# Kernel optimization log

Measured on AMD Instinct MI355X. Metric: run time of the kernel, lower is better.

## Reference

```python
import jax, jax.numpy as jnp
import numpy as np

EMBED_DIM = 512
NUM_HEADS = 8
HEAD_DIM = EMBED_DIM // NUM_HEADS
SCALE = HEAD_DIM ** -0.5


def setup_inputs() -> dict:
    key = jax.random.key(0)
    ks = jax.random.split(key, 12)
    B, Nq, Nk, C = 2, 2048, 2048, EMBED_DIM
    # xavier_uniform bound for square CxC weights
    bound = float(np.sqrt(6.0 / (C + C)))
    def w(k):
        return jax.random.uniform(k, (C, C), jnp.float32, -bound, bound)
    return {
        "query": jax.random.normal(ks[0], (B, Nq, C), jnp.float32),
        "key": jax.random.normal(ks[1], (B, Nk, C), jnp.float32),
        "value": jax.random.normal(ks[2], (B, Nk, C), jnp.float32),
        "key_padding_mask": jnp.zeros((B, Nk), dtype=bool),
        "Wq": w(ks[3]), "bq": jnp.zeros((C,), jnp.float32),
        "Wk": w(ks[4]), "bk": jnp.zeros((C,), jnp.float32),
        "Wv": w(ks[5]), "bv": jnp.zeros((C,), jnp.float32),
        "Wo": w(ks[6]), "bo": jnp.zeros((C,), jnp.float32),
    }


def reference(query, key, value, key_padding_mask, Wq, bq, Wk, bk, Wv, bv, Wo, bo):
    B, Nq, C = query.shape
    Nk = key.shape[1]
    H, D = NUM_HEADS, HEAD_DIM
    # torch Linear: x @ W.T + b
    Q = (query @ Wq.T + bq).reshape(B, Nq, H, D).transpose(0, 2, 1, 3)  # (B,H,Nq,D)
    K = (key @ Wk.T + bk).reshape(B, Nk, H, D).transpose(0, 2, 1, 3)
    V = (value @ Wv.T + bv).reshape(B, Nk, H, D).transpose(0, 2, 1, 3)
    scores = jnp.einsum("bhqd,bhkd->bhqk", Q, K) * SCALE  # (B,H,Nq,Nk)
    scores = jnp.where(key_padding_mask[:, None, None, :], -jnp.inf, scores)
    attn = jax.nn.softmax(scores, axis=-1)
    out = jnp.einsum("bhqk,bhkd->bhqd", attn, V)  # (B,H,Nq,D)
    out = out.transpose(0, 2, 1, 3).reshape(B, Nq, C)
    return out @ Wo.T + bo
```

## Files before the change

### kernel.cpp

```cpp
#include <hip/hip_runtime.h>

typedef unsigned short u16;
typedef __attribute__((ext_vector_type(8))) short short8;
typedef __attribute__((ext_vector_type(8))) __bf16 bf16x8;
typedef __attribute__((ext_vector_type(4))) float f32x4;
typedef __attribute__((ext_vector_type(4))) unsigned int u32x4;

#define MFMA_BF16(a, b, c) __builtin_amdgcn_mfma_f32_16x16x32_bf16((a), (b), (c), 0, 0, 0)

__device__ __forceinline__ u16 f2bf(float f) {
    unsigned u = __builtin_bit_cast(unsigned, f);
    u += 0x7FFFu + ((u >> 16) & 1u);
    return (u16)(u >> 16);
}

__device__ __forceinline__ unsigned cvt_pk_bf16(float lo, float hi) {
    unsigned r;
    asm("v_cvt_pk_bf16_f32 %0, %1, %2" : "=v"(r) : "v"(lo), "v"(hi));
    return r;
}

__device__ __forceinline__ float fast_exp2(float x) {
    float r;
    asm("v_exp_f32 %0, %1" : "=v"(r) : "v"(x));
    return r;
}

__global__ __launch_bounds__(256) void proj_gemm(
    const float* __restrict__ Xq, const float* __restrict__ Xk, const float* __restrict__ Xv,
    const float* __restrict__ Wq, const float* __restrict__ Wk, const float* __restrict__ Wv,
    const float* __restrict__ bq, const float* __restrict__ bk, const float* __restrict__ bv,
    u16* __restrict__ Oq, u16* __restrict__ Ok, u16* __restrict__ Ov)
{
    constexpr int K = 512, N = 512;
    const int z = blockIdx.z;
    const float* __restrict__ X = (z == 0) ? Xq : (z == 1) ? Xk : Xv;
    const float* __restrict__ W = (z == 0) ? Wq : (z == 1) ? Wk : Wv;
    const float* __restrict__ bias = (z == 0) ? bq : (z == 1) ? bk : bv;
    u16* __restrict__ O = (z == 0) ? Oq : (z == 1) ? Ok : Ov;
    const float alpha = (z == 0) ? 0.125f * 1.44269504088896f : 1.0f;

    __shared__ u16 lA[128 * 64];
    __shared__ u16 lB[128 * 64];

    const int tid = threadIdx.x, lane = tid & 63, w = tid >> 6;
    const int wr = w >> 1, wc = w & 1;
    const int bm = blockIdx.x, bn = blockIdx.y;
    const int r0 = tid >> 3, cc = tid & 7;

    f32x4 acc[4][4];
    for (int m = 0; m < 4; ++m)
        for (int n = 0; n < 4; ++n)
            acc[m][n] = f32x4{0.f, 0.f, 0.f, 0.f};

    for (int kt = 0; kt < K; kt += 64) {
        __syncthreads();
        for (int p = 0; p < 4; ++p) {
            int r = r0 + p * 32;
            {
                const float4* g = (const float4*)(X + (size_t)(bm * 128 + r) * K + kt + cc * 8);
                float4 f0 = g[0], f1 = g[1];
                short8 v;
                v[0] = (short)f2bf(f0.x); v[1] = (short)f2bf(f0.y);
                v[2] = (short)f2bf(f0.z); v[3] = (short)f2bf(f0.w);
                v[4] = (short)f2bf(f1.x); v[5] = (short)f2bf(f1.y);
                v[6] = (short)f2bf(f1.z); v[7] = (short)f2bf(f1.w);
                *(short8*)&lA[r * 64 + ((cc ^ (r & 7)) << 3)] = v;
            }
            {
                const float4* g = (const float4*)(W + (size_t)(bn * 128 + r) * K + kt + cc * 8);
                float4 f0 = g[0], f1 = g[1];
                short8 v;
                v[0] = (short)f2bf(f0.x); v[1] = (short)f2bf(f0.y);
                v[2] = (short)f2bf(f0.z); v[3] = (short)f2bf(f0.w);
                v[4] = (short)f2bf(f1.x); v[5] = (short)f2bf(f1.y);
                v[6] = (short)f2bf(f1.z); v[7] = (short)f2bf(f1.w);
                *(short8*)&lB[r * 64 + ((cc ^ (r & 7)) << 3)] = v;
            }
        }
        __syncthreads();
        for (int kk = 0; kk < 2; ++kk) {
            bf16x8 af[4], bfr[4];
            for (int m = 0; m < 4; ++m) {
                int row = wr * 64 + m * 16 + (lane & 15);
                af[m] = *(const bf16x8*)&lA[row * 64 + (((kk * 4 + (lane >> 4)) ^ (row & 7)) << 3)];
            }
            for (int n = 0; n < 4; ++n) {
                int row = wc * 64 + n * 16 + (lane & 15);
                bfr[n] = *(const bf16x8*)&lB[row * 64 + (((kk * 4 + (lane >> 4)) ^ (row & 7)) << 3)];
            }
            for (int m = 0; m < 4; ++m)
                for (int n = 0; n < 4; ++n)
                    acc[m][n] = MFMA_BF16(af[m], bfr[n], acc[m][n]);
        }
    }
    for (int m = 0; m < 4; ++m)
        for (int n = 0; n < 4; ++n) {
            int row = bm * 128 + wr * 64 + m * 16 + ((lane >> 4) << 2);
            int col = bn * 128 + wc * 64 + n * 16 + (lane & 15);
            float bv_ = bias[col];
            for (int i = 0; i < 4; ++i) {
                float v = (acc[m][n][i] + bv_) * alpha;
                O[(size_t)(row + i) * N + col] = f2bf(v);
            }
        }
}

__global__ __launch_bounds__(256) void out_gemm(
    const u16* __restrict__ A, const float* __restrict__ W,
    const float* __restrict__ bias, float* __restrict__ O)
{
    constexpr int K = 512, N = 512;
    __shared__ u16 lA[128 * 64];
    __shared__ u16 lB[128 * 64];

    const int tid = threadIdx.x, lane = tid & 63, w = tid >> 6;
    const int wr = w >> 1, wc = w & 1;
    const int bm = blockIdx.x, bn = blockIdx.y;
    const int r0 = tid >> 3, cc = tid & 7;

    f32x4 acc[4][4];
    for (int m = 0; m < 4; ++m)
        for (int n = 0; n < 4; ++n)
            acc[m][n] = f32x4{0.f, 0.f, 0.f, 0.f};

    for (int kt = 0; kt < K; kt += 64) {
        __syncthreads();
        for (int p = 0; p < 4; ++p) {
            int r = r0 + p * 32;
            *(short8*)&lA[r * 64 + ((cc ^ (r & 7)) << 3)] =
                *(const short8*)(A + (size_t)(bm * 128 + r) * K + kt + cc * 8);
            const float4* g = (const float4*)(W + (size_t)(bn * 128 + r) * K + kt + cc * 8);
            float4 f0 = g[0], f1 = g[1];
            short8 v;
            v[0] = (short)f2bf(f0.x); v[1] = (short)f2bf(f0.y);
            v[2] = (short)f2bf(f0.z); v[3] = (short)f2bf(f0.w);
            v[4] = (short)f2bf(f1.x); v[5] = (short)f2bf(f1.y);
            v[6] = (short)f2bf(f1.z); v[7] = (short)f2bf(f1.w);
            *(short8*)&lB[r * 64 + ((cc ^ (r & 7)) << 3)] = v;
        }
        __syncthreads();
        for (int kk = 0; kk < 2; ++kk) {
            bf16x8 af[4], bfr[4];
            for (int m = 0; m < 4; ++m) {
                int row = wr * 64 + m * 16 + (lane & 15);
                af[m] = *(const bf16x8*)&lA[row * 64 + (((kk * 4 + (lane >> 4)) ^ (row & 7)) << 3)];
            }
            for (int n = 0; n < 4; ++n) {
                int row = wc * 64 + n * 16 + (lane & 15);
                bfr[n] = *(const bf16x8*)&lB[row * 64 + (((kk * 4 + (lane >> 4)) ^ (row & 7)) << 3)];
            }
            for (int m = 0; m < 4; ++m)
                for (int n = 0; n < 4; ++n)
                    acc[m][n] = MFMA_BF16(af[m], bfr[n], acc[m][n]);
        }
    }
    for (int m = 0; m < 4; ++m)
        for (int n = 0; n < 4; ++n) {
            int row = bm * 128 + wr * 64 + m * 16 + ((lane >> 4) << 2);
            int col = bn * 128 + wc * 64 + n * 16 + (lane & 15);
            float bv_ = bias[col];
            for (int i = 0; i < 4; ++i)
                O[(size_t)(row + i) * N + col] = acc[m][n][i] + bv_;
        }
}

__global__ __launch_bounds__(512, 2) void attn_k(
    const u16* __restrict__ Qp, const u16* __restrict__ Kp, const u16* __restrict__ Vp,
    const unsigned char* __restrict__ mask, u16* __restrict__ Ob)
{
    constexpr int C = 512, NK = 2048, KVH = 1024, NTG = KVH / 64;
    __shared__ u16 lK[2][64 * 64];
    __shared__ u16 lV[2][64 * 64];

    const int tid = threadIdx.x, lane = tid & 63, w = tid >> 6;
    const int g = w >> 2, wg = w & 3;
    const int gd = lane >> 4, q15 = lane & 15;
    const int bh = blockIdx.x, qb = blockIdx.y;
    const int b = bh >> 3, h = bh & 7;
    const size_t qrow0 = (size_t)b * 2048 + qb * 64;
    const size_t krow0 = (size_t)b * 2048;
    const int col0 = h * 64;
    const int rs = tid >> 3, cc = tid & 7;

    bf16x8 qf[2];
    {
        const u16* qrow = Qp + (qrow0 + wg * 16 + q15) * C + col0;
        qf[0] = *(const bf16x8*)(qrow + gd * 8);
        qf[1] = *(const bf16x8*)(qrow + 32 + gd * 8);
    }

    float mst = -1e30f, lstp = 0.f;
    f32x4 oacc[4];
    #pragma unroll
    for (int i = 0; i < 4; ++i) oacc[i] = f32x4{0.f, 0.f, 0.f, 0.f};

    short8 kreg[2], vreg[2];
    #pragma unroll
    for (int g2 = 0; g2 < 2; ++g2) {
        kreg[g2] = *(const short8*)(Kp + (krow0 + g2 * KVH + rs) * C + col0 + cc * 8);
        vreg[g2] = *(const short8*)(Vp + (krow0 + g2 * KVH + rs) * C + col0 + cc * 8);
    }

    for (int t = 0; t < NTG; ++t) {
        __syncthreads();
        #pragma unroll
        for (int g2 = 0; g2 < 2; ++g2) {
            *(short8*)&lK[g2][rs * 64 + ((cc ^ (rs & 7)) << 3)] = kreg[g2];
            #pragma unroll
            for (int j = 0; j < 8; ++j)
                lV[g2][(cc * 8 + j) * 64 + (((rs >> 3) ^ ((j + cc) & 7)) << 3) + (rs & 7)] = (u16)vreg[g2][j];
        }
        if (t + 1 < NTG) {
            #pragma unroll
            for (int g2 = 0; g2 < 2; ++g2) {
                const size_t row = krow0 + g2 * KVH + (t + 1) * 64 + rs;
                kreg[g2] = *(const short8*)(Kp + row * C + col0 + cc * 8);
                vreg[g2] = *(const short8*)(Vp + row * C + col0 + cc * 8);
            }
        }
        __syncthreads();

        unsigned char mby = mask[(size_t)b * NK + g * KVH + t * 64 + lane];

        f32x4 s[4];
        #pragma unroll
        for (int i = 0; i < 4; ++i) s[i] = f32x4{0.f, 0.f, 0.f, 0.f};
        const u16* Kc = &lK[g][0];
        __builtin_amdgcn_s_setprio(1);
        #pragma unroll
        for (int kb = 0; kb < 2; ++kb)
            #pragma unroll
            for (int t4 = 0; t4 < 4; ++t4) {
                int krow = t4 * 16 + q15;
                bf16x8 kf = *(const bf16x8*)&Kc[krow * 64 + (((kb * 4 + gd) ^ (krow & 7)) << 3)];
                s[t4] = MFMA_BF16(kf, qf[kb], s[t4]);
            }
        __builtin_amdgcn_s_setprio(0);

        unsigned long long m64 = __ballot(mby != 0);
        if (m64) {
            #pragma unroll
            for (int t4 = 0; t4 < 4; ++t4)
                #pragma unroll
                for (int i = 0; i < 4; ++i) {
                    int k = t4 * 16 + gd * 4 + i;
                    if ((m64 >> k) & 1ull) s[t4][i] = -1e30f;
                }
        }

        float pmax = s[0][0];
        #pragma unroll
        for (int t4 = 0; t4 < 4; ++t4)
            #pragma unroll
            for (int i = 0; i < 4; ++i) pmax = fmaxf(pmax, s[t4][i]);

        if (!__all(pmax - mst <= 11.0f)) {
            float rm = fmaxf(pmax, __shfl_xor(pmax, 16));
            rm = fmaxf(rm, __shfl_xor(rm, 32));
            float mn = fmaxf(mst, rm);
            float sf = exp2f(mst - mn);
            mst = mn;
            lstp *= sf;
            #pragma unroll
            for (int i = 0; i < 4; ++i) {
                float sfi = __shfl(sf, (lane & 48) | ((gd << 2) + i));
                #pragma unroll
                for (int t2 = 0; t2 < 4; ++t2) oacc[t2][i] *= sfi;
            }
        }

        const u16* Vc = &lV[g][0];
        float rsum = 0.f;
        #pragma unroll
        for (int kb = 0; kb < 2; ++kb) {
            float ea[4], eb[4];
            #pragma unroll
            for (int i = 0; i < 4; ++i) {
                ea[i] = fast_exp2(s[2 * kb][i] - mst);
                eb[i] = fast_exp2(s[2 * kb + 1][i] - mst);
                rsum += ea[i] + eb[i];
            }
            u32x4 pw;
            pw[0] = cvt_pk_bf16(ea[0], ea[1]);
            pw[1] = cvt_pk_bf16(ea[2], ea[3]);
            pw[2] = cvt_pk_bf16(eb[0], eb[1]);
            pw[3] = cvt_pk_bf16(eb[2], eb[3]);
            bf16x8 pa = __builtin_bit_cast(bf16x8, pw);
            __builtin_amdgcn_s_setprio(1);
            #pragma unroll
            for (int t2 = 0; t2 < 4; ++t2) {
                int d = t2 * 16 + q15;
                int swd = (d + (d >> 3)) & 7;
                int base = d * 64 + 4 * (gd & 1);
                uint2 v0 = *(const uint2*)&Vc[base + (((4 * kb + 0 + (gd >> 1)) ^ swd) << 3)];
                uint2 v1 = *(const uint2*)&Vc[base + (((4 * kb + 2 + (gd >> 1)) ^ swd) << 3)];
                u32x4 vw; vw[0] = v0.x; vw[1] = v0.y; vw[2] = v1.x; vw[3] = v1.y;
                bf16x8 vf = __builtin_bit_cast(bf16x8, vw);
                oacc[t2] = MFMA_BF16(pa, vf, oacc[t2]);
            }
            __builtin_amdgcn_s_setprio(0);
        }
        lstp += rsum;
    }

    float lsum = lstp + __shfl_xor(lstp, 16);
    lsum += __shfl_xor(lsum, 32);

    __syncthreads();

    float* mrg = (float*)&lK[0][0];
    const int mbase = (wg * 64 + lane) * 18;
    if (g == 1) {
        #pragma unroll
        for (int t2 = 0; t2 < 4; ++t2)
            #pragma unroll
            for (int i = 0; i < 4; ++i) mrg[mbase + t2 * 4 + i] = oacc[t2][i];
        mrg[mbase + 16] = mst;
        mrg[mbase + 17] = lsum;
    }
    __syncthreads();
    if (g == 0) {
        float mst1 = mrg[mbase + 16], ls1 = mrg[mbase + 17];
        float m = fmaxf(mst, mst1);
        float a0 = exp2f(mst - m), a1 = exp2f(mst1 - m);
        float lr = lsum * a0 + ls1 * a1;
        #pragma unroll
        for (int i = 0; i < 4; ++i) {
            int srcl = (lane & 48) | ((gd << 2) + i);
            float a0i = __shfl(a0, srcl), a1i = __shfl(a1, srcl), li = __shfl(lr, srcl);
            float inv = 1.f / li;
            int qg = qb * 64 + wg * 16 + gd * 4 + i;
            #pragma unroll
            for (int t2 = 0; t2 < 4; ++t2) {
                float o1 = mrg[mbase + t2 * 4 + i];
                float vfin = (oacc[t2][i] * a0i + o1 * a1i) * inv;
                Ob[((size_t)b * 2048 + qg) * C + col0 + t2 * 16 + q15] = f2bf(vfin);
            }
        }
    }
}

extern "C" void kernel_launch(void* const* d_in, const int* in_sizes, int n_in,
                              void* d_out, int out_size, void* d_ws, size_t ws_size,
                              hipStream_t stream) {
    const float* query = (const float*)d_in[0];
    const float* key   = (const float*)d_in[1];
    const float* value = (const float*)d_in[2];
    const unsigned char* mask = (const unsigned char*)d_in[3];
    const float* Wq = (const float*)d_in[4];
    const float* bq = (const float*)d_in[5];
    const float* Wk = (const float*)d_in[6];
    const float* bk = (const float*)d_in[7];
    const float* Wv = (const float*)d_in[8];
    const float* bv = (const float*)d_in[9];
    const float* Wo = (const float*)d_in[10];
    const float* bo = (const float*)d_in[11];

    u16* ws = (u16*)d_ws;
    u16* Qp = ws;
    u16* Kp = ws + 2097152;
    u16* Vp = ws + 4194304;
    u16* Ob = ws + 6291456;

    dim3 gp(32, 4, 3);
    proj_gemm<<<gp, 256, 0, stream>>>(query, key, value, Wq, Wk, Wv, bq, bk, bv, Qp, Kp, Vp);

    dim3 ga(16, 32);
    attn_k<<<ga, 512, 0, stream>>>(Qp, Kp, Vp, mask, Ob);

    dim3 go(32, 4);
    out_gemm<<<go, 256, 0, stream>>>(Ob, Wo, bo, (float*)d_out);
}
```

Baseline: 80.50 us.

## Halve attention block threads; each wave processes two 16-row query tiles

The attention kernel drops from 512 to 256 threads per block, and each wave now handles two 16-row query sub-tiles (A and B). Each K fragment read from LDS feeds two MFMAs, and each V fragment does the same, which halves LDS read traffic per unit of compute. The V transpose into LDS is rewritten to pack pairs of bf16 values and store them as 64-bit words instead of scalar 16-bit stores. In exchange each thread holds twice the accumulators and softmax state, raising register pressure and possibly cutting occupancy, and each block has fewer waves to hide latency.

```diff
diff --git a/kernel.cpp b/kernel.cpp
--- a/kernel.cpp
+++ b/kernel.cpp
@@ -165,7 +165,7 @@
         }
 }
 
-__global__ __launch_bounds__(512, 2) void attn_k(
+__global__ __launch_bounds__(256) void attn_k(
     const u16* __restrict__ Qp, const u16* __restrict__ Kp, const u16* __restrict__ Vp,
     const unsigned char* __restrict__ mask, u16* __restrict__ Ob)
 {
@@ -174,58 +174,76 @@
     __shared__ u16 lV[2][64 * 64];
 
     const int tid = threadIdx.x, lane = tid & 63, w = tid >> 6;
-    const int g = w >> 2, wg = w & 3;
+    const int g = w >> 1, wg = w & 1;
     const int gd = lane >> 4, q15 = lane & 15;
     const int bh = blockIdx.x, qb = blockIdx.y;
     const int b = bh >> 3, h = bh & 7;
     const size_t qrow0 = (size_t)b * 2048 + qb * 64;
-    const size_t krow0 = (size_t)b * 2048;
+    const size_t krow0 = (size_t)b * 2048 + (size_t)g * KVH;
     const int col0 = h * 64;
-    const int rs = tid >> 3, cc = tid & 7;
-
-    bf16x8 qf[2];
+    const int gt = tid & 127;
+    const int rs8 = gt >> 3, cc = gt & 7;
+
+    bf16x8 qfA[2], qfB[2];
     {
-        const u16* qrow = Qp + (qrow0 + wg * 16 + q15) * C + col0;
-        qf[0] = *(const bf16x8*)(qrow + gd * 8);
-        qf[1] = *(const bf16x8*)(qrow + 32 + gd * 8);
-    }
-
-    float mst = -1e30f, lstp = 0.f;
-    f32x4 oacc[4];
+        const u16* qa = Qp + (qrow0 + wg * 32 + q15) * C + col0;
+        qfA[0] = *(const bf16x8*)(qa + gd * 8);
+        qfA[1] = *(const bf16x8*)(qa + 32 + gd * 8);
+        const u16* qbp = qa + 16 * C;
+        qfB[0] = *(const bf16x8*)(qbp + gd * 8);
+        qfB[1] = *(const bf16x8*)(qbp + 32 + gd * 8);
+    }
+
+    float mstA = -1e30f, lstA = 0.f, mstB = -1e30f, lstB = 0.f;
+    f32x4 oaccA[4], oaccB[4];
     #pragma unroll
-    for (int i = 0; i < 4; ++i) oacc[i] = f32x4{0.f, 0.f, 0.f, 0.f};
-
-    short8 kreg[2], vreg[2];
+    for (int i = 0; i < 4; ++i) {
+        oaccA[i] = f32x4{0.f, 0.f, 0.f, 0.f};
+        oaccB[i] = f32x4{0.f, 0.f, 0.f, 0.f};
+    }
+
+    short8 kpre[4], vpre[4];
     #pragma unroll
-    for (int g2 = 0; g2 < 2; ++g2) {
-        kreg[g2] = *(const short8*)(Kp + (krow0 + g2 * KVH + rs) * C + col0 + cc * 8);
-        vreg[g2] = *(const short8*)(Vp + (krow0 + g2 * KVH + rs) * C + col0 + cc * 8);
-    }
+    for (int p = 0; p < 4; ++p)
+        kpre[p] = *(const short8*)(Kp + (krow0 + rs8 + p * 16) * C + col0 + cc * 8);
+    #pragma unroll
+    for (int j = 0; j < 4; ++j)
+        vpre[j] = *(const short8*)(Vp + (krow0 + 4 * rs8 + j) * C + col0 + cc * 8);
 
     for (int t = 0; t < NTG; ++t) {
         __syncthreads();
         #pragma unroll
-        for (int g2 = 0; g2 < 2; ++g2) {
-            *(short8*)&lK[g2][rs * 64 + ((cc ^ (rs & 7)) << 3)] = kreg[g2];
-            #pragma unroll
-            for (int j = 0; j < 8; ++j)
-                lV[g2][(cc * 8 + j) * 64 + (((rs >> 3) ^ ((j + cc) & 7)) << 3) + (rs & 7)] = (u16)vreg[g2][j];
+        for (int p = 0; p < 4; ++p) {
+            int r = rs8 + p * 16;
+            *(short8*)&lK[g][r * 64 + ((cc ^ (r & 7)) << 3)] = kpre[p];
+        }
+        #pragma unroll
+        for (int jj = 0; jj < 8; ++jj) {
+            int d = cc * 8 + jj;
+            int swd = (d + (d >> 3)) & 7;
+            unsigned w0 = ((unsigned)(u16)vpre[0][jj]) | (((unsigned)(u16)vpre[1][jj]) << 16);
+            unsigned w1 = ((unsigned)(u16)vpre[2][jj]) | (((unsigned)(u16)vpre[3][jj]) << 16);
+            uint2 pr; pr.x = w0; pr.y = w1;
+            *(uint2*)&lV[g][d * 64 + (((rs8 >> 1) ^ swd) << 3) + 4 * (rs8 & 1)] = pr;
         }
         if (t + 1 < NTG) {
             #pragma unroll
-            for (int g2 = 0; g2 < 2; ++g2) {
-                const size_t row = krow0 + g2 * KVH + (t + 1) * 64 + rs;
-                kreg[g2] = *(const short8*)(Kp + row * C + col0 + cc * 8);
-                vreg[g2] = *(const short8*)(Vp + row * C + col0 + cc * 8);
-            }
+            for (int p = 0; p < 4; ++p)
+                kpre[p] = *(const short8*)(Kp + (krow0 + (t + 1) * 64 + rs8 + p * 16) * C + col0 + cc * 8);
+            #pragma unroll
+            for (int j = 0; j < 4; ++j)
+                vpre[j] = *(const short8*)(Vp + (krow0 + (t + 1) * 64 + 4 * rs8 + j) * C + col0 + cc * 8);
         }
         __syncthreads();
 
         unsigned char mby = mask[(size_t)b * NK + g * KVH + t * 64 + lane];
 
-        f32x4 s[4];
-        #pragma unroll
-        for (int i = 0; i < 4; ++i) s[i] = f32x4{0.f, 0.f, 0.f, 0.f};
+        f32x4 sA[4], sB[4];
+        #pragma unroll
+        for (int i = 0; i < 4; ++i) {
+            sA[i] = f32x4{0.f, 0.f, 0.f, 0.f};
+            sB[i] = f32x4{0.f, 0.f, 0.f, 0.f};
+        }
         const u16* Kc = &lK[g][0];
         __builtin_amdgcn_s_setprio(1);
         #pragma unroll
@@ -234,7 +252,8 @@
             for (int t4 = 0; t4 < 4; ++t4) {
                 int krow = t4 * 16 + q15;
                 bf16x8 kf = *(const bf16x8*)&Kc[krow * 64 + (((kb * 4 + gd) ^ (krow & 7)) << 3)];
-                s[t4] = MFMA_BF16(kf, qf[kb], s[t4]);
+                sA[t4] = MFMA_BF16(kf, qfA[kb], sA[t4]);
+                sB[t4] = MFMA_BF16(kf, qfB[kb], sB[t4]);
             }
         __builtin_amdgcn_s_setprio(0);
 
@@ -245,49 +264,92 @@
                 #pragma unroll
                 for (int i = 0; i < 4; ++i) {
                     int k = t4 * 16 + gd * 4 + i;
-                    if ((m64 >> k) & 1ull) s[t4][i] = -1e30f;
-                }
-        }
-
-        float pmax = s[0][0];
-        #pragma unroll
-        for (int t4 = 0; t4 < 4; ++t4)
-            #pragma unroll
-            for (int i = 0; i < 4; ++i) pmax = fmaxf(pmax, s[t4][i]);
-
-        if (!__all(pmax - mst <= 11.0f)) {
-            float rm = fmaxf(pmax, __shfl_xor(pmax, 16));
-            rm = fmaxf(rm, __shfl_xor(rm, 32));
-            float mn = fmaxf(mst, rm);
-            float sf = exp2f(mst - mn);
-            mst = mn;
-            lstp *= sf;
-            #pragma unroll
-            for (int i = 0; i < 4; ++i) {
-                float sfi = __shfl(sf, (lane & 48) | ((gd << 2) + i));
-                #pragma unroll
-                for (int t2 = 0; t2 < 4; ++t2) oacc[t2][i] *= sfi;
-            }
+                    if ((m64 >> k) & 1ull) { sA[t4][i] = -1e30f; sB[t4][i] = -1e30f; }
+                }
+        }
+
+        bf16x8 paA[2], paB[2];
+        {
+            float pmax = sA[0][0];
+            #pragma unroll
+            for (int t4 = 0; t4 < 4; ++t4)
+                #pragma unroll
+                for (int i = 0; i < 4; ++i) pmax = fmaxf(pmax, sA[t4][i]);
+            if (!__all(pmax - mstA <= 11.0f)) {
+                float rm = fmaxf(pmax, __shfl_xor(pmax, 16));
+                rm = fmaxf(rm, __shfl_xor(rm, 32));
+                float mn = fmaxf(mstA, rm);
+                float sf = exp2f(mstA - mn);
+                mstA = mn; lstA *= sf;
+                #pragma unroll
+                for (int i = 0; i < 4; ++i) {
+                    float sfi = __shfl(sf, (lane & 48) | ((gd << 2) + i));
+                    #pragma unroll
+                    for (int t2 = 0; t2 < 4; ++t2) oaccA[t2][i] *= sfi;
+                }
+            }
+            float rsum = 0.f;
+            #pragma unroll
+            for (int kb = 0; kb < 2; ++kb) {
+                float ea[4], eb[4];
+                #pragma unroll
+                for (int i = 0; i < 4; ++i) {
+                    ea[i] = fast_exp2(sA[2 * kb][i] - mstA);
+                    eb[i] = fast_exp2(sA[2 * kb + 1][i] - mstA);
+                    rsum += ea[i] + eb[i];
+                }
+                u32x4 pw;
+                pw[0] = cvt_pk_bf16(ea[0], ea[1]);
+                pw[1] = cvt_pk_bf16(ea[2], ea[3]);
+                pw[2] = cvt_pk_bf16(eb[0], eb[1]);
+                pw[3] = cvt_pk_bf16(eb[2], eb[3]);
+                paA[kb] = __builtin_bit_cast(bf16x8, pw);
+            }
+            lstA += rsum;
+        }
+        {
+            float pmax = sB[0][0];
+            #pragma unroll
+            for (int t4 = 0; t4 < 4; ++t4)
+                #pragma unroll
+                for (int i = 0; i < 4; ++i) pmax = fmaxf(pmax, sB[t4][i]);
+            if (!__all(pmax - mstB <= 11.0f)) {
+                float rm = fmaxf(pmax, __shfl_xor(pmax, 16));
+                rm = fmaxf(rm, __shfl_xor(rm, 32));
+                float mn = fmaxf(mstB, rm);
+                float sf = exp2f(mstB - mn);
+                mstB = mn; lstB *= sf;
+                #pragma unroll
+                for (int i = 0; i < 4; ++i) {
+                    float sfi = __shfl(sf, (lane & 48) | ((gd << 2) + i));
+                    #pragma unroll
+                    for (int t2 = 0; t2 < 4; ++t2) oaccB[t2][i] *= sfi;
+                }
+            }
+            float rsum = 0.f;
+            #pragma unroll
+            for (int kb = 0; kb < 2; ++kb) {
+                float ea[4], eb[4];
+                #pragma unroll
+                for (int i = 0; i < 4; ++i) {
+                    ea[i] = fast_exp2(sB[2 * kb][i] - mstB);
+                    eb[i] = fast_exp2(sB[2 * kb + 1][i] - mstB);
+                    rsum += ea[i] + eb[i];
+                }
+                u32x4 pw;
+                pw[0] = cvt_pk_bf16(ea[0], ea[1]);
+                pw[1] = cvt_pk_bf16(ea[2], ea[3]);
+                pw[2] = cvt_pk_bf16(eb[0], eb[1]);
+                pw[3] = cvt_pk_bf16(eb[2], eb[3]);
+                paB[kb] = __builtin_bit_cast(bf16x8, pw);
+            }
+            lstB += rsum;
         }
 
         const u16* Vc = &lV[g][0];
-        float rsum = 0.f;
-        #pragma unroll
-        for (int kb = 0; kb < 2; ++kb) {
-            float ea[4], eb[4];
-            #pragma unroll
-            for (int i = 0; i < 4; ++i) {
-                ea[i] = fast_exp2(s[2 * kb][i] - mst);
-                eb[i] = fast_exp2(s[2 * kb + 1][i] - mst);
-                rsum += ea[i] + eb[i];
-            }
-            u32x4 pw;
-            pw[0] = cvt_pk_bf16(ea[0], ea[1]);
-            pw[1] = cvt_pk_bf16(ea[2], ea[3]);
-            pw[2] = cvt_pk_bf16(eb[0], eb[1]);
-            pw[3] = cvt_pk_bf16(eb[2], eb[3]);
-            bf16x8 pa = __builtin_bit_cast(bf16x8, pw);
-            __builtin_amdgcn_s_setprio(1);
+        __builtin_amdgcn_s_setprio(1);
+        #pragma unroll
+        for (int kb = 0; kb < 2; ++kb)
             #pragma unroll
             for (int t2 = 0; t2 < 4; ++t2) {
                 int d = t2 * 16 + q15;
@@ -297,45 +359,69 @@
                 uint2 v1 = *(const uint2*)&Vc[base + (((4 * kb + 2 + (gd >> 1)) ^ swd) << 3)];
                 u32x4 vw; vw[0] = v0.x; vw[1] = v0.y; vw[2] = v1.x; vw[3] = v1.y;
                 bf16x8 vf = __builtin_bit_cast(bf16x8, vw);
-                oacc[t2] = MFMA_BF16(pa, vf, oacc[t2]);
-            }
-            __builtin_amdgcn_s_setprio(0);
-        }
-        lstp += rsum;
-    }
-
-    float lsum = lstp + __shfl_xor(lstp, 16);
-    lsum += __shfl_xor(lsum, 32);
+                oaccA[t2] = MFMA_BF16(paA[kb], vf, oaccA[t2]);
+                oaccB[t2] = MFMA_BF16(paB[kb], vf, oaccB[t2]);
+            }
+        __builtin_amdgcn_s_setprio(0);
+    }
+
+    float lsA = lstA + __shfl_xor(lstA, 16); lsA += __shfl_xor(lsA, 32);
+    float lsB = lstB + __shfl_xor(lstB, 16); lsB += __shfl_xor(lsB, 32);
 
     __syncthreads();
 
     float* mrg = (float*)&lK[0][0];
-    const int mbase = (wg * 64 + lane) * 18;
+    const int recA = ((wg * 2 + 0) * 64 + lane) * 18;
+    const int recB = ((wg * 2 + 1) * 64 + lane) * 18;
     if (g == 1) {
         #pragma unroll
         for (int t2 = 0; t2 < 4; ++t2)
             #pragma unroll
-            for (int i = 0; i < 4; ++i) mrg[mbase + t2 * 4 + i] = oacc[t2][i];
-        mrg[mbase + 16] = mst;
-        mrg[mbase + 17] = lsum;
+            for (int i = 0; i < 4; ++i) {
+                mrg[recA + t2 * 4 + i] = oaccA[t2][i];
+                mrg[recB + t2 * 4 + i] = oaccB[t2][i];
+            }
+        mrg[recA + 16] = mstA; mrg[recA + 17] = lsA;
+        mrg[recB + 16] = mstB; mrg[recB + 17] = lsB;
     }
     __syncthreads();
     if (g == 0) {
-        float mst1 = mrg[mbase + 16], ls1 = mrg[mbase + 17];
-        float m = fmaxf(mst, mst1);
-        float a0 = exp2f(mst - m), a1 = exp2f(mst1 - m);
-        float lr = lsum * a0 + ls1 * a1;
-        #pragma unroll
-        for (int i = 0; i < 4; ++i) {
-            int srcl = (lane & 48) | ((gd << 2) + i);
-            float a0i = __shfl(a0, srcl), a1i = __shfl(a1, srcl), li = __shfl(lr, srcl);
-            float inv = 1.f / li;
-            int qg = qb * 64 + wg * 16 + gd * 4 + i;
-            #pragma unroll
-            for (int t2 = 0; t2 < 4; ++t2) {
-                float o1 = mrg[mbase + t2 * 4 + i];
-                float vfin = (oacc[t2][i] * a0i + o1 * a1i) * inv;
-                Ob[((size_t)b * 2048 + qg) * C + col0 + t2 * 16 + q15] = f2bf(vfin);
+        {
+            float m1 = mrg[recA + 16], l1 = mrg[recA + 17];
+            float m = fmaxf(mstA, m1);
+            float a0 = exp2f(mstA - m), a1 = exp2f(m1 - m);
+            float lr = lsA * a0 + l1 * a1;
+            #pragma unroll
+            for (int i = 0; i < 4; ++i) {
+                int srcl = (lane & 48) | ((gd << 2) + i);
+                float a0i = __shfl(a0, srcl), a1i = __shfl(a1, srcl), li = __shfl(lr, srcl);
+                float inv = 1.f / li;
+                int qg = qb * 64 + wg * 32 + gd * 4 + i;
+                #pragma unroll
+                for (int t2 = 0; t2 < 4; ++t2) {
+                    float o1 = mrg[recA + t2 * 4 + i];
+                    float vfin = (oaccA[t2][i] * a0i + o1 * a1i) * inv;
+                    Ob[((size_t)b * 2048 + qg) * C + col0 + t2 * 16 + q15] = f2bf(vfin);
+                }
+            }
+        }
+        {
+            float m1 = mrg[recB + 16], l1 = mrg[recB + 17];
+            float m = fmaxf(mstB, m1);
+            float a0 = exp2f(mstB - m), a1 = exp2f(m1 - m);
+            float lr = lsB * a0 + l1 * a1;
+            #pragma unroll
+            for (int i = 0; i < 4; ++i) {
+                int srcl = (lane & 48) | ((gd << 2) + i);
+                float a0i = __shfl(a0, srcl), a1i = __shfl(a1, srcl), li = __shfl(lr, srcl);
+                float inv = 1.f / li;
+                int qg = qb * 64 + wg * 32 + 16 + gd * 4 + i;
+                #pragma unroll
+                for (int t2 = 0; t2 < 4; ++t2) {
+                    float o1 = mrg[recB + t2 * 4 + i];
+                    float vfin = (oaccB[t2][i] * a0i + o1 * a1i) * inv;
+                    Ob[((size_t)b * 2048 + qg) * C + col0 + t2 * 16 + q15] = f2bf(vfin);
+                }
             }
         }
     }
@@ -367,7 +453,7 @@
     proj_gemm<<<gp, 256, 0, stream>>>(query, key, value, Wq, Wk, Wv, bq, bk, bv, Qp, Kp, Vp);
 
     dim3 ga(16, 32);
-    attn_k<<<ga, 512, 0, stream>>>(Qp, Kp, Vp, mask, Ob);
+    attn_k<<<ga, 256, 0, stream>>>(Qp, Kp, Vp, mask, Ob);
 
     dim3 go(32, 4);
     out_gemm<<<go, 256, 0, stream>>>(Ob, Wo, bo, (float*)d_out);
```

Measured after the change: 91.72 us. +13.9%, slower.
